# Optimization experiments

Measured on AMD Instinct MI355X. Metric: run time of the kernel, lower is better.

The kernel has to match this reference:

```python
import jax, jax.numpy as jnp
import numpy as np

N, E, F, H, K = 20000, 640000, 128, 128, 2


def setup_inputs() -> dict:
    key = jax.random.key(0)
    ks = jax.random.split(key, 8)
    x = jax.random.normal(ks[0], (N, F), jnp.float32)
    src = jax.random.randint(ks[1], (E,), 0, N)
    dst = jax.random.randint(ks[2], (E,), 0, N)
    edge_weight = jax.random.uniform(ks[3], (E,), jnp.float32)
    h = jnp.zeros((N, H), jnp.float32)
    c = jnp.zeros((N, H), jnp.float32)
    Wx = jax.random.normal(ks[4], (4, K, F, H), jnp.float32) * 0.05
    Wh = jax.random.normal(ks[5], (4, K, H, H), jnp.float32) * 0.05
    b = jnp.zeros((4, H), jnp.float32)
    wc = jax.random.normal(ks[6], (3, H), jnp.float32) * 0.05
    return dict(x=x, edge_weight=edge_weight, h=h, c=c, Wx=Wx, Wh=Wh, b=b, wc=wc,
                src=src, dst=dst)


def _lhat(x, src, dst, w_sym, n):
    # Scaled Laplacian (sym norm, lambda_max=2): L_hat = L - I = -D^-1/2 A D^-1/2
    return -jax.ops.segment_sum(w_sym[:, None] * x[src], dst, num_segments=n)


def _cheb(x, W, src, dst, w_sym, n):
    # Chebyshev recursion: T0=x, T1=L_hat x, Tk = 2 L_hat T_{k-1} - T_{k-2}
    Tx0 = x
    out = Tx0 @ W[0]
    if W.shape[0] > 1:
        Tx1 = _lhat(x, src, dst, w_sym, n)
        out = out + Tx1 @ W[1]
        for k in range(2, W.shape[0]):
            Tx2 = 2.0 * _lhat(Tx1, src, dst, w_sym, n) - Tx0
            out = out + Tx2 @ W[k]
            Tx0, Tx1 = Tx1, Tx2
    return out


def reference(x, edge_weight, h, c, Wx, Wh, b, wc, src, dst):
    n = x.shape[0]
    # symmetric normalization of edge weights
    deg = jax.ops.segment_sum(edge_weight, src, num_segments=n)
    dis = jnp.where(deg > 0, jax.lax.rsqrt(jnp.maximum(deg, 1e-12)), 0.0)
    w_sym = dis[src] * edge_weight * dis[dst]

    gx = lambda W: _cheb(x, W, src, dst, w_sym, n)
    gh = lambda W: _cheb(h, W, src, dst, w_sym, n)

    i = jax.nn.sigmoid(gx(Wx[0]) + gh(Wh[0]) + wc[0] * c + b[0])
    f = jax.nn.sigmoid(gx(Wx[1]) + gh(Wh[1]) + wc[1] * c + b[1])
    c_new = f * c + i * jnp.tanh(gx(Wx[2]) + gh(Wh[2]) + b[2])
    o = jax.nn.sigmoid(gx(Wx[3]) + gh(Wh[3]) + wc[2] * c_new + b[3])
    h_new = o * jnp.tanh(c_new)
    # module returns (out, h, c) with out == new hidden state
    return h_new, h_new, c_new
```

## Files before the change

### kernel.cpp

```cpp
#include <hip/hip_runtime.h>
#include <math.h>

#define FD 128
#define GATES 4
#define NB   128
#define NRH  2
#define NRF  2
#define RSH_MAX 10016
#define RSF_MAX 10016
#define NMAX (RSH_MAX * 2)

typedef __attribute__((ext_vector_type(8))) short bf16x8;
typedef __attribute__((ext_vector_type(4))) float f32x4;

__device__ __forceinline__ float sigmoidf_(float v) {
    return 1.0f / (1.0f + expf(-v));
}

__device__ __forceinline__ unsigned short f2bf(float f) {
    unsigned int u = __builtin_bit_cast(unsigned int, f);
    u += 0x7fffu + ((u >> 16) & 1u);
    return (unsigned short)(u >> 16);
}
__device__ __forceinline__ float bflo(unsigned int u) {
    return __builtin_bit_cast(float, u << 16);
}
__device__ __forceinline__ float bfhi(unsigned int u) {
    return __builtin_bit_cast(float, u & 0xffff0000u);
}
__device__ __forceinline__ unsigned int pack2bf(float lo, float hi) {
    return (unsigned int)f2bf(lo) | ((unsigned int)f2bf(hi) << 16);
}

__global__ __launch_bounds__(512) void k_front(
    const float* __restrict__ ew, const int* __restrict__ src,
    const int* __restrict__ dst,
    float* __restrict__ deg_priv, unsigned short* __restrict__ cnt_priv,
    int* __restrict__ cursor, int* __restrict__ hflag,
    const float* __restrict__ x, const float* __restrict__ h,
    const float* __restrict__ Wx, const float* __restrict__ Wh,
    unsigned int* __restrict__ xw, unsigned int* __restrict__ hw,
    unsigned short* __restrict__ Abf, unsigned short* __restrict__ Wbf,
    int* __restrict__ flagpart,
    int E, int n, int ech, int rs, int n16, int cvb) {

    __shared__ float        degL[RSH_MAX];
    __shared__ unsigned int cntP[RSH_MAX / 2];

    const int bid  = blockIdx.x;
    const int tid  = threadIdx.x;
    const int lane = tid & 63;
    const int NH_BLOCKS = NB * NRH;

    if (bid < NH_BLOCKS) {
        if (bid == 0 && tid == 0) { cursor[0] = 0; hflag[0] = 0; }

        const int b    = bid & (NB - 1);
        const int r    = bid >> 7;
        const int base = r * rs;
        const int rse  = min(rs, n - base);
        const int nh   = (rse + 1) >> 1;

        for (int i = tid; i < rse; i += 512) degL[i] = 0.f;
        for (int i = tid; i < nh;  i += 512) cntP[i] = 0u;
        __syncthreads();

        const int e0 = b * ech, e1 = min(e0 + ech, E);
        for (int e = e0 + tid; e < e1; e += 512) {
            int s = src[e], d = dst[e];
            unsigned int rs_ = (unsigned int)(s - base);
            unsigned int rd_ = (unsigned int)(d - base);
            if (rs_ < (unsigned int)rse) atomicAdd(&degL[rs_], ew[e]);
            if (rd_ < (unsigned int)rse) atomicAdd(&cntP[rd_ >> 1], (rd_ & 1) ? 0x10000u : 1u);
        }
        __syncthreads();

        float*          dp = deg_priv + (size_t)b * n + base;
        unsigned short* cp = cnt_priv + (size_t)b * n + base;
        for (int i = tid; i < rse; i += 512) dp[i] = degL[i];
        for (int i = tid; i < rse; i += 512) {
            unsigned int v = cntP[i >> 1];
            cp[i] = (unsigned short)((i & 1) ? (v >> 16) : (v & 0xffffu));
        }
        return;
    }

    if (bid < NH_BLOCKS + cvb) {
        int t = (bid - NH_BLOCKS) * 512 + tid;
        bool nz = false;
        if (t < n16) {
            int r = t >> 4, o = t & 15;
            int slot = ((r & 15) + 16 * (o & 3)) * 8;
            size_t fb = ((size_t)(r >> 4) * 16) * 512;

            const float4* xp = reinterpret_cast<const float4*>(x) + (size_t)t * 2;
            float4 a = xp[0], bq = xp[1];
            uint4 ox;
            ox.x = pack2bf(a.x, a.y);   ox.y = pack2bf(a.z, a.w);
            ox.z = pack2bf(bq.x, bq.y); ox.w = pack2bf(bq.z, bq.w);
            reinterpret_cast<uint4*>(xw)[t] = ox;
            *reinterpret_cast<uint4*>(Abf + fb + (size_t)(o >> 2) * 512 + slot) = ox;

            const float4* hp = reinterpret_cast<const float4*>(h) + (size_t)t * 2;
            float4 hc = hp[0], hd = hp[1];
            nz = (hc.x != 0.f) | (hc.y != 0.f) | (hc.z != 0.f) | (hc.w != 0.f) |
                 (hd.x != 0.f) | (hd.y != 0.f) | (hd.z != 0.f) | (hd.w != 0.f);
            uint4 oh;
            oh.x = pack2bf(hc.x, hc.y); oh.y = pack2bf(hc.z, hc.w);
            oh.z = pack2bf(hd.x, hd.y); oh.w = pack2bf(hd.z, hd.w);
            reinterpret_cast<uint4*>(hw)[t] = oh;
            *reinterpret_cast<uint4*>(Abf + fb + (size_t)(8 + (o >> 2)) * 512 + slot) = oh;
        }
        __shared__ int fsh;
        if (tid == 0) fsh = 0;
        __syncthreads();
        unsigned long long m = __ballot(nz);
        if (lane == 0 && m) atomicOr(&fsh, 1);
        __syncthreads();
        if (tid == 0) flagpart[bid - NH_BLOCKS] = fsh;
        return;
    }

    {
        int frag = (bid - NH_BLOCKS - cvb) * 8 + (tid >> 6);
        int cb = frag >> 4, kb = frag & 15;
        int col = cb * 16 + (lane & 15);
        int k0  = kb * 32 + (lane >> 4) * 8;

        int sel  = k0 >> 7;
        int g    = col >> 7;
        int j    = col & (FD - 1);
        const float* Wb = (sel < 2) ? Wx : Wh;
        const float* p = Wb + (((size_t)g * 2 + (sel & 1)) * FD + (k0 & (FD - 1))) * FD + j;

        unsigned short outv[8];
        #pragma unroll
        for (int i = 0; i < 8; ++i) outv[i] = f2bf(p[(size_t)i * FD]);
        *reinterpret_cast<uint4*>(Wbf + (size_t)frag * 512 + lane * 8) =
            *reinterpret_cast<uint4*>(outv);
    }
}

__global__ __launch_bounds__(512) void k_fold(
    const float* __restrict__ deg_priv, const unsigned short* __restrict__ cnt_priv,
    float* __restrict__ dis, int* __restrict__ cnt, int* __restrict__ off,
    int* __restrict__ curb, int* __restrict__ cursor, int n) {

    __shared__ float degp[4][128];
    __shared__ int   ctp[4][128];
    __shared__ int   offL[128];

    const int tid = threadIdx.x;
    const int seg = tid >> 7;
    const int dl  = tid & 127;
    const int d   = blockIdx.x * 128 + dl;
    const int b0  = seg * 32;

    float s = 0.f; int ct = 0;
    if (d < n) {
        #pragma unroll 8
        for (int i = 0; i < 32; ++i) {
            int b = b0 + i;
            s  += deg_priv[(size_t)b * n + d];
            ct += (int)cnt_priv[(size_t)b * n + d];
        }
    }
    degp[seg][dl] = s;
    ctp[seg][dl]  = ct;
    __syncthreads();

    if (seg == 0) {
        int   ctt = 0;
        float st  = 0.f;
        #pragma unroll
        for (int q = 0; q < 4; ++q) { ctt += ctp[q][dl]; st += degp[q][dl]; }

        const int lane = tid & 63;
        int s_incl = (d < n) ? ctt : 0;
        #pragma unroll
        for (int o = 1; o < 64; o <<= 1) {
            int t2 = __shfl_up(s_incl, o);
            if (lane >= o) s_incl += t2;
        }
        int wtotal = __shfl(s_incl, 63);
        int base = 0;
        if (lane == 0) base = atomicAdd(cursor, wtotal);
        base = __shfl(base, 0);

        if (d < n) {
            dis[d] = (st > 0.0f) ? rsqrtf(fmaxf(st, 1e-12f)) : 0.0f;
            cnt[d] = ctt;
            int my0 = base + s_incl - ((d < n) ? ctt : 0);
            off[d]   = my0;
            offL[dl] = my0;
        }
    }
    __syncthreads();

    if (d < n) {
        int run = offL[dl];
        for (int q = 0; q < seg; ++q) run += ctp[q][dl];
        #pragma unroll 8
        for (int i = 0; i < 32; ++i) {
            int b = b0 + i;
            curb[(size_t)b * n + d] = run;
            run += (int)cnt_priv[(size_t)b * n + d];
        }
    }
}

__global__ __launch_bounds__(512) void k_fill_lds(
    const float* __restrict__ ew, const int* __restrict__ src,
    const int* __restrict__ dst, const float* __restrict__ dis,
    const int* __restrict__ curb, int2* __restrict__ epk,
    const int* __restrict__ flagpart, int* __restrict__ hflag,
    int E, int n, int ech, int rs, int cvb) {

    __shared__ int curL[RSF_MAX];

    const int b    = blockIdx.x & (NB - 1);
    const int r    = blockIdx.x >> 7;
    const int base = r * rs;
    const int rse  = min(rs, n - base);

    if (blockIdx.x == 0) {
        int fl = 0;
        for (int i = threadIdx.x; i < cvb; i += 512) fl |= flagpart[i];
        unsigned long long m = __ballot(fl != 0);
        if ((threadIdx.x & 63) == 0 && m) atomicOr(hflag, 1);
    }

    const int* crow = curb + (size_t)b * n + base;
    for (int i = threadIdx.x; i < rse; i += 512) curL[i] = crow[i];
    __syncthreads();

    const int e0 = b * ech, e1 = min(e0 + ech, E);
    for (int e = e0 + (int)threadIdx.x; e < e1; e += 512) {
        int d = dst[e];
        unsigned int rd_ = (unsigned int)(d - base);
        if (rd_ < (unsigned int)rse) {
            int s = src[e];
            float w = -dis[s] * ew[e] * dis[d];
            int p = atomicAdd(&curL[rd_], 1);
            epk[p] = make_int2(s, __builtin_bit_cast(int, w));
        }
    }
}

__global__ __launch_bounds__(256) void k_gather_bf(
    const unsigned int* __restrict__ xw, const unsigned int* __restrict__ hw,
    const int* __restrict__ off, const int* __restrict__ cntv,
    const int2* __restrict__ epk, const int* __restrict__ hflag,
    unsigned short* __restrict__ Abf, int n) {

    int d    = blockIdx.x * 4 + (threadIdx.x >> 6);
    int lane = threadIdx.x & 63;
    if (d >= n) return;
    const bool hasH = (*hflag) != 0;

    int p0 = off[d], p1 = p0 + cntv[d];
    float ax0 = 0.f, ax1 = 0.f, ah0 = 0.f, ah1 = 0.f;

    if (!hasH) {
        for (int base = p0; base < p1; base += 64) {
            int cnt = min(64, p1 - base);
            int2 my = make_int2(0, 0);
            if (lane < cnt) my = epk[base + lane];
            int   sm = my.x;
            float wm = __builtin_bit_cast(float, my.y);
            int k = 0;
            for (; k + 4 <= cnt; k += 4) {
                int   s0 = __shfl(sm, k),     s1 = __shfl(sm, k + 1);
                int   s2 = __shfl(sm, k + 2), s3 = __shfl(sm, k + 3);
                float w0 = __shfl(wm, k),     w1 = __shfl(wm, k + 1);
                float w2 = __shfl(wm, k + 2), w3 = __shfl(wm, k + 3);
                unsigned int u0 = xw[s0 * 64 + lane];
                unsigned int u1 = xw[s1 * 64 + lane];
                unsigned int u2 = xw[s2 * 64 + lane];
                unsigned int u3 = xw[s3 * 64 + lane];
                ax0 = fmaf(w0, bflo(u0), ax0); ax1 = fmaf(w0, bfhi(u0), ax1);
                ax0 = fmaf(w1, bflo(u1), ax0); ax1 = fmaf(w1, bfhi(u1), ax1);
                ax0 = fmaf(w2, bflo(u2), ax0); ax1 = fmaf(w2, bfhi(u2), ax1);
                ax0 = fmaf(w3, bflo(u3), ax0); ax1 = fmaf(w3, bfhi(u3), ax1);
            }
            for (; k < cnt; ++k) {
                int s = __shfl(sm, k);
                float w = __shfl(wm, k);
                unsigned int u = xw[s * 64 + lane];
                ax0 = fmaf(w, bflo(u), ax0); ax1 = fmaf(w, bfhi(u), ax1);
            }
        }
    } else {
        for (int base = p0; base < p1; base += 64) {
            int cnt = min(64, p1 - base);
            int2 my = make_int2(0, 0);
            if (lane < cnt) my = epk[base + lane];
            int   sm = my.x;
            float wm = __builtin_bit_cast(float, my.y);
            int k = 0;
            for (; k + 2 <= cnt; k += 2) {
                int   s0 = __shfl(sm, k), s1 = __shfl(sm, k + 1);
                float w0 = __shfl(wm, k), w1 = __shfl(wm, k + 1);
                unsigned int u0 = xw[s0 * 64 + lane];
                unsigned int v0 = hw[s0 * 64 + lane];
                unsigned int u1 = xw[s1 * 64 + lane];
                unsigned int v1 = hw[s1 * 64 + lane];
                ax0 = fmaf(w0, bflo(u0), ax0); ax1 = fmaf(w0, bfhi(u0), ax1);
                ah0 = fmaf(w0, bflo(v0), ah0); ah1 = fmaf(w0, bfhi(v0), ah1);
                ax0 = fmaf(w1, bflo(u1), ax0); ax1 = fmaf(w1, bfhi(u1), ax1);
                ah0 = fmaf(w1, bflo(v1), ah0); ah1 = fmaf(w1, bfhi(v1), ah1);
            }
            for (; k < cnt; ++k) {
                int s = __shfl(sm, k);
                float w = __shfl(wm, k);
                unsigned int u = xw[s * 64 + lane];
                unsigned int v = hw[s * 64 + lane];
                ax0 = fmaf(w, bflo(u), ax0); ax1 = fmaf(w, bfhi(u), ax1);
                ah0 = fmaf(w, bflo(v), ah0); ah1 = fmaf(w, bfhi(v), ah1);
            }
        }
    }

    unsigned int* Au = (unsigned int*)Abf;
    size_t fragT = (size_t)(d >> 4) * 16 + 4 + (lane >> 4);
    int slotu = ((d & 15) + 16 * ((lane >> 2) & 3)) * 4 + (lane & 3);
    Au[fragT * 256 + slotu] = pack2bf(ax0, ax1);
    if (hasH) Au[(fragT + 8) * 256 + slotu] = pack2bf(ah0, ah1);
}

__global__ __launch_bounds__(512) void k_gemm_lstm(
    const unsigned short* __restrict__ Abf, const unsigned short* __restrict__ Wbf,
    const int* __restrict__ hflag,
    const float* __restrict__ c, const float* __restrict__ bias,
    const float* __restrict__ wc, float* __restrict__ out, int n) {

    int rt   = blockIdx.x;
    int jj   = threadIdx.x >> 6;
    int lane = threadIdx.x & 63;
    const int kbmax = (*hflag) ? 16 : 8;

    f32x4 acc[4][4];
    #pragma unroll
    for (int mi = 0; mi < 4; ++mi)
        #pragma unroll
        for (int g = 0; g < 4; ++g)
            acc[mi][g] = (f32x4)0.0f;

    const size_t aoff = ((size_t)(rt * 4) * 16) * 512 + lane * 8;

    for (int kb = 0; kb < kbmax; ++kb) {
        bf16x8 a[4], b[4];
        #pragma unroll
        for (int mi = 0; mi < 4; ++mi)
            a[mi] = *reinterpret_cast<const bf16x8*>(Abf + aoff + (size_t)(mi * 16 + kb) * 512);
        #pragma unroll
        for (int g = 0; g < 4; ++g)
            b[g] = *reinterpret_cast<const bf16x8*>(
                Wbf + ((size_t)(g * 8 + jj) * 16 + kb) * 512 + lane * 8);
        #pragma unroll
        for (int mi = 0; mi < 4; ++mi)
            #pragma unroll
            for (int g = 0; g < 4; ++g)
                acc[mi][g] = __builtin_amdgcn_mfma_f32_16x16x32_bf16(
                                 a[mi], b[g], acc[mi][g], 0, 0, 0);
    }

    const int r0   = rt * 64;
    const int col  = jj * 16 + (lane & 15);
    const size_t NH = (size_t)n * FD;
    const float wc0 = wc[0 * FD + col], wc1 = wc[1 * FD + col], wc2 = wc[2 * FD + col];
    const float b0  = bias[0 * FD + col], b1 = bias[1 * FD + col];
    const float b2  = bias[2 * FD + col], b3 = bias[3 * FD + col];

    #pragma unroll
    for (int mi = 0; mi < 4; ++mi) {
        #pragma unroll
        for (int q = 0; q < 4; ++q) {
            int r = r0 + mi * 16 + (lane >> 4) * 4 + q;
            if (r >= n) continue;
            float cv = c[(size_t)r * FD + col];
            float gi = acc[mi][0][q] + wc0 * cv + b0;
            float gf = acc[mi][1][q] + wc1 * cv + b1;
            float gg = acc[mi][2][q] + b2;
            float iv = sigmoidf_(gi);
            float fv = sigmoidf_(gf);
            float cn = fv * cv + iv * tanhf(gg);
            float go = acc[mi][3][q] + wc2 * cn + b3;
            float hn = sigmoidf_(go) * tanhf(cn);
            size_t o = (size_t)r * FD + col;
            out[o]          = hn;
            out[NH + o]     = hn;
            out[2 * NH + o] = cn;
        }
    }
}

extern "C" void kernel_launch(void* const* d_in, const int* in_sizes, int n_in,
                              void* d_out, int out_size, void* d_ws, size_t ws_size,
                              hipStream_t stream) {
    const float* x   = (const float*)d_in[0];
    const float* ew  = (const float*)d_in[1];
    const float* h   = (const float*)d_in[2];
    const float* c   = (const float*)d_in[3];
    const float* Wx  = (const float*)d_in[4];
    const float* Wh  = (const float*)d_in[5];
    const float* b   = (const float*)d_in[6];
    const float* wc  = (const float*)d_in[7];
    const int*   src = (const int*)d_in[8];
    const int*   dst = (const int*)d_in[9];

    const int n = in_sizes[0] / FD;
    const int E = in_sizes[1];

    const int Mpad = (n + 63) & ~63;
    const int ech  = (E + NB - 1) / NB;
    const int rsh  = (n + NRH - 1) / NRH;
    const int rsf  = (n + NRF - 1) / NRF;
    const int n16  = n * 16;
    const int cvb  = (n16 + 511) / 512;
    const int npf  = (n + 127) / 128;

    float* dis      = (float*)d_ws;
    int*   cnt      = (int*)(dis + n);
    int*   off      = cnt + n;
    int*   hflag    = off + n + 4;
    int*   cursor   = hflag + 4;
    int*   flagpart = cursor + 4;
    int2*  epk      = (int2*)(flagpart + 1280);
    unsigned int* xw = (unsigned int*)(epk + E);
    unsigned int* hw = xw + (size_t)n * 64;
    unsigned short* Abf = (unsigned short*)(hw + (size_t)n * 64);
    unsigned short* Wbf = Abf + (size_t)Mpad * 512;
    int*   curb     = (int*)(Wbf + 512 * 512);
    float* deg_priv = (float*)(curb + (size_t)NB * n);
    unsigned short* cnt_priv = (unsigned short*)(deg_priv + (size_t)NB * n);

    k_front<<<NB * NRH + cvb + 64, 512, 0, stream>>>(
        ew, src, dst, deg_priv, cnt_priv, cursor, hflag,
        x, h, Wx, Wh, xw, hw, Abf, Wbf, flagpart,
        E, n, ech, rsh, n16, cvb);
    k_fold<<<npf, 512, 0, stream>>>(deg_priv, cnt_priv, dis, cnt, off, curb,
                                    cursor, n);
    k_fill_lds<<<NB * NRF, 512, 0, stream>>>(ew, src, dst, dis, curb, epk,
                                             flagpart, hflag, E, n, ech, rsf, cvb);
    k_gather_bf<<<(n + 3) / 4, 256, 0, stream>>>(xw, hw, off, cnt, epk, hflag, Abf, n);

    k_gemm_lstm<<<Mpad / 64, 512, 0, stream>>>(Abf, Wbf, hflag, c, b, wc,
                                               (float*)d_out, n);
}
```

Measured before the change: 95.13 us.

## Stage GEMM A operand through LDS from row-major bf16 buffers

```diff
diff --git a/kernel.cpp b/kernel.cpp
--- a/kernel.cpp
+++ b/kernel.cpp
@@ -9,6 +9,7 @@
 #define RSH_MAX 10016
 #define RSF_MAX 10016
 #define NMAX (RSH_MAX * 2)
+#define LDW 68
 
 typedef __attribute__((ext_vector_type(8))) short bf16x8;
 typedef __attribute__((ext_vector_type(4))) float f32x4;
@@ -40,8 +41,7 @@
     const float* __restrict__ x, const float* __restrict__ h,
     const float* __restrict__ Wx, const float* __restrict__ Wh,
     unsigned int* __restrict__ xw, unsigned int* __restrict__ hw,
-    unsigned short* __restrict__ Abf, unsigned short* __restrict__ Wbf,
-    int* __restrict__ flagpart,
+    unsigned short* __restrict__ Wbf, int* __restrict__ flagpart,
     int E, int n, int ech, int rs, int n16, int cvb) {
 
     __shared__ float        degL[RSH_MAX];
@@ -66,7 +66,21 @@
         __syncthreads();
 
         const int e0 = b * ech, e1 = min(e0 + ech, E);
-        for (int e = e0 + tid; e < e1; e += 512) {
+        int e = e0 + tid * 2;
+        for (; e + 1 < e1; e += 1024) {
+            int2   s2 = *reinterpret_cast<const int2*>(src + e);
+            int2   d2 = *reinterpret_cast<const int2*>(dst + e);
+            float2 w2 = *reinterpret_cast<const float2*>(ew + e);
+            unsigned int rs0 = (unsigned int)(s2.x - base);
+            unsigned int rd0 = (unsigned int)(d2.x - base);
+            unsigned int rs1 = (unsigned int)(s2.y - base);
+            unsigned int rd1 = (unsigned int)(d2.y - base);
+            if (rs0 < (unsigned int)rse) atomicAdd(&degL[rs0], w2.x);
+            if (rd0 < (unsigned int)rse) atomicAdd(&cntP[rd0 >> 1], (rd0 & 1) ? 0x10000u : 1u);
+            if (rs1 < (unsigned int)rse) atomicAdd(&degL[rs1], w2.y);
+            if (rd1 < (unsigned int)rse) atomicAdd(&cntP[rd1 >> 1], (rd1 & 1) ? 0x10000u : 1u);
+        }
+        if (e < e1) {
             int s = src[e], d = dst[e];
             unsigned int rs_ = (unsigned int)(s - base);
             unsigned int rd_ = (unsigned int)(d - base);
@@ -89,17 +103,12 @@
         int t = (bid - NH_BLOCKS) * 512 + tid;
         bool nz = false;
         if (t < n16) {
-            int r = t >> 4, o = t & 15;
-            int slot = ((r & 15) + 16 * (o & 3)) * 8;
-            size_t fb = ((size_t)(r >> 4) * 16) * 512;
-
             const float4* xp = reinterpret_cast<const float4*>(x) + (size_t)t * 2;
             float4 a = xp[0], bq = xp[1];
             uint4 ox;
             ox.x = pack2bf(a.x, a.y);   ox.y = pack2bf(a.z, a.w);
             ox.z = pack2bf(bq.x, bq.y); ox.w = pack2bf(bq.z, bq.w);
             reinterpret_cast<uint4*>(xw)[t] = ox;
-            *reinterpret_cast<uint4*>(Abf + fb + (size_t)(o >> 2) * 512 + slot) = ox;
 
             const float4* hp = reinterpret_cast<const float4*>(h) + (size_t)t * 2;
             float4 hc = hp[0], hd = hp[1];
@@ -109,7 +118,6 @@
             oh.x = pack2bf(hc.x, hc.y); oh.y = pack2bf(hc.z, hc.w);
             oh.z = pack2bf(hd.x, hd.y); oh.w = pack2bf(hd.z, hd.w);
             reinterpret_cast<uint4*>(hw)[t] = oh;
-            *reinterpret_cast<uint4*>(Abf + fb + (size_t)(8 + (o >> 2)) * 512 + slot) = oh;
         }
         __shared__ int fsh;
         if (tid == 0) fsh = 0;
@@ -190,7 +198,7 @@
         if (d < n) {
             dis[d] = (st > 0.0f) ? rsqrtf(fmaxf(st, 1e-12f)) : 0.0f;
             cnt[d] = ctt;
-            int my0 = base + s_incl - ((d < n) ? ctt : 0);
+            int my0 = base + s_incl - ctt;
             off[d]   = my0;
             offL[dl] = my0;
         }
@@ -235,7 +243,25 @@
     __syncthreads();
 
     const int e0 = b * ech, e1 = min(e0 + ech, E);
-    for (int e = e0 + (int)threadIdx.x; e < e1; e += 512) {
+    int e = e0 + (int)threadIdx.x * 2;
+    for (; e + 1 < e1; e += 1024) {
+        int2   s2 = *reinterpret_cast<const int2*>(src + e);
+        int2   d2 = *reinterpret_cast<const int2*>(dst + e);
+        float2 w2 = *reinterpret_cast<const float2*>(ew + e);
+        unsigned int rd0 = (unsigned int)(d2.x - base);
+        if (rd0 < (unsigned int)rse) {
+            float w = -dis[s2.x] * w2.x * dis[d2.x];
+            int p = atomicAdd(&curL[rd0], 1);
+            epk[p] = make_int2(s2.x, __builtin_bit_cast(int, w));
+        }
+        unsigned int rd1 = (unsigned int)(d2.y - base);
+        if (rd1 < (unsigned int)rse) {
+            float w = -dis[s2.y] * w2.y * dis[d2.y];
+            int p = atomicAdd(&curL[rd1], 1);
+            epk[p] = make_int2(s2.y, __builtin_bit_cast(int, w));
+        }
+    }
+    if (e < e1) {
         int d = dst[e];
         unsigned int rd_ = (unsigned int)(d - base);
         if (rd_ < (unsigned int)rse) {
@@ -251,7 +277,7 @@
     const unsigned int* __restrict__ xw, const unsigned int* __restrict__ hw,
     const int* __restrict__ off, const int* __restrict__ cntv,
     const int2* __restrict__ epk, const int* __restrict__ hflag,
-    unsigned short* __restrict__ Abf, int n) {
+    unsigned int* __restrict__ txw, unsigned int* __restrict__ thw, int n) {
 
     int d    = blockIdx.x * 4 + (threadIdx.x >> 6);
     int lane = threadIdx.x & 63;
@@ -290,6 +316,7 @@
                 ax0 = fmaf(w, bflo(u), ax0); ax1 = fmaf(w, bfhi(u), ax1);
             }
         }
+        txw[(size_t)d * 64 + lane] = pack2bf(ax0, ax1);
     } else {
         for (int base = p0; base < p1; base += 64) {
             int cnt = min(64, p1 - base);
@@ -319,25 +346,27 @@
                 ah0 = fmaf(w, bflo(v), ah0); ah1 = fmaf(w, bfhi(v), ah1);
             }
         }
-    }
-
-    unsigned int* Au = (unsigned int*)Abf;
-    size_t fragT = (size_t)(d >> 4) * 16 + 4 + (lane >> 4);
-    int slotu = ((d & 15) + 16 * ((lane >> 2) & 3)) * 4 + (lane & 3);
-    Au[fragT * 256 + slotu] = pack2bf(ax0, ax1);
-    if (hasH) Au[(fragT + 8) * 256 + slotu] = pack2bf(ah0, ah1);
+        txw[(size_t)d * 64 + lane] = pack2bf(ax0, ax1);
+        thw[(size_t)d * 64 + lane] = pack2bf(ah0, ah1);
+    }
 }
 
 __global__ __launch_bounds__(512) void k_gemm_lstm(
-    const unsigned short* __restrict__ Abf, const unsigned short* __restrict__ Wbf,
-    const int* __restrict__ hflag,
+    const unsigned int* __restrict__ xw, const unsigned int* __restrict__ txw,
+    const unsigned int* __restrict__ hw, const unsigned int* __restrict__ thw,
+    const unsigned short* __restrict__ Wbf, const int* __restrict__ hflag,
     const float* __restrict__ c, const float* __restrict__ bias,
     const float* __restrict__ wc, float* __restrict__ out, int n) {
 
-    int rt   = blockIdx.x;
-    int jj   = threadIdx.x >> 6;
-    int lane = threadIdx.x & 63;
-    const int kbmax = (*hflag) ? 16 : 8;
+    __shared__ unsigned int ldsR[64][LDW];
+    __shared__ unsigned int ldsG[64][LDW];
+
+    const int rt   = blockIdx.x;
+    const int tid  = threadIdx.x;
+    const int jj   = tid >> 6;
+    const int lane = tid & 63;
+    const int r0   = rt * 64;
+    const bool hasH = (*hflag) != 0;
 
     f32x4 acc[4][4];
     #pragma unroll
@@ -346,13 +375,33 @@
         for (int g = 0; g < 4; ++g)
             acc[mi][g] = (f32x4)0.0f;
 
-    const size_t aoff = ((size_t)(rt * 4) * 16) * 512 + lane * 8;
-
-    for (int kb = 0; kb < kbmax; ++kb) {
+    {
+        int sr = tid >> 3, sc = (tid & 7) * 8;
+        uint4 v0 = make_uint4(0,0,0,0), v1 = make_uint4(0,0,0,0);
+        uint4 g0 = make_uint4(0,0,0,0), g1 = make_uint4(0,0,0,0);
+        if (r0 + sr < n) {
+            const uint4* p = reinterpret_cast<const uint4*>(xw + (size_t)(r0 + sr) * 64 + sc);
+            v0 = p[0]; v1 = p[1];
+            const uint4* q = reinterpret_cast<const uint4*>(txw + (size_t)(r0 + sr) * 64 + sc);
+            g0 = q[0]; g1 = q[1];
+        }
+        *reinterpret_cast<uint4*>(&ldsR[sr][sc])     = v0;
+        *reinterpret_cast<uint4*>(&ldsR[sr][sc + 4]) = v1;
+        *reinterpret_cast<uint4*>(&ldsG[sr][sc])     = g0;
+        *reinterpret_cast<uint4*>(&ldsG[sr][sc + 4]) = g1;
+    }
+    __syncthreads();
+
+    #pragma unroll
+    for (int kb = 0; kb < 8; ++kb) {
         bf16x8 a[4], b[4];
-        #pragma unroll
-        for (int mi = 0; mi < 4; ++mi)
-            a[mi] = *reinterpret_cast<const bf16x8*>(Abf + aoff + (size_t)(mi * 16 + kb) * 512);
+        const int c0 = (kb & 3) * 16 + (lane >> 4) * 4;
+        #pragma unroll
+        for (int mi = 0; mi < 4; ++mi) {
+            const unsigned int* lp = (kb < 4) ? &ldsR[mi * 16 + (lane & 15)][c0]
+                                              : &ldsG[mi * 16 + (lane & 15)][c0];
+            a[mi] = __builtin_bit_cast(bf16x8, *reinterpret_cast<const uint4*>(lp));
+        }
         #pragma unroll
         for (int g = 0; g < 4; ++g)
             b[g] = *reinterpret_cast<const bf16x8*>(
@@ -365,7 +414,49 @@
                                  a[mi], b[g], acc[mi][g], 0, 0, 0);
     }
 
-    const int r0   = rt * 64;
+    if (hasH) {
+        __syncthreads();
+        {
+            int sr = tid >> 3, sc = (tid & 7) * 8;
+            uint4 v0 = make_uint4(0,0,0,0), v1 = make_uint4(0,0,0,0);
+            uint4 g0 = make_uint4(0,0,0,0), g1 = make_uint4(0,0,0,0);
+            if (r0 + sr < n) {
+                const uint4* p = reinterpret_cast<const uint4*>(hw + (size_t)(r0 + sr) * 64 + sc);
+                v0 = p[0]; v1 = p[1];
+                const uint4* q = reinterpret_cast<const uint4*>(thw + (size_t)(r0 + sr) * 64 + sc);
+                g0 = q[0]; g1 = q[1];
+            }
+            *reinterpret_cast<uint4*>(&ldsR[sr][sc])     = v0;
+            *reinterpret_cast<uint4*>(&ldsR[sr][sc + 4]) = v1;
+            *reinterpret_cast<uint4*>(&ldsG[sr][sc])     = g0;
+            *reinterpret_cast<uint4*>(&ldsG[sr][sc + 4]) = g1;
+        }
+        __syncthreads();
+
+        #pragma unroll
+        for (int kk = 0; kk < 8; ++kk) {
+            const int kb = 8 + kk;
+            bf16x8 a[4], b[4];
+            const int c0 = (kk & 3) * 16 + (lane >> 4) * 4;
+            #pragma unroll
+            for (int mi = 0; mi < 4; ++mi) {
+                const unsigned int* lp = (kk < 4) ? &ldsR[mi * 16 + (lane & 15)][c0]
+                                                  : &ldsG[mi * 16 + (lane & 15)][c0];
+                a[mi] = __builtin_bit_cast(bf16x8, *reinterpret_cast<const uint4*>(lp));
+            }
+            #pragma unroll
+            for (int g = 0; g < 4; ++g)
+                b[g] = *reinterpret_cast<const bf16x8*>(
+                    Wbf + ((size_t)(g * 8 + jj) * 16 + kb) * 512 + lane * 8);
+            #pragma unroll
+            for (int mi = 0; mi < 4; ++mi)
+                #pragma unroll
+                for (int g = 0; g < 4; ++g)
+                    acc[mi][g] = __builtin_amdgcn_mfma_f32_16x16x32_bf16(
+                                     a[mi], b[g], acc[mi][g], 0, 0, 0);
+        }
+    }
+
     const int col  = jj * 16 + (lane & 15);
     const size_t NH = (size_t)n * FD;
     const float wc0 = wc[0 * FD + col], wc1 = wc[1 * FD + col], wc2 = wc[2 * FD + col];
@@ -427,24 +518,25 @@
     int*   cursor   = hflag + 4;
     int*   flagpart = cursor + 4;
     int2*  epk      = (int2*)(flagpart + 1280);
-    unsigned int* xw = (unsigned int*)(epk + E);
-    unsigned int* hw = xw + (size_t)n * 64;
-    unsigned short* Abf = (unsigned short*)(hw + (size_t)n * 64);
-    unsigned short* Wbf = Abf + (size_t)Mpad * 512;
+    unsigned int* xw  = (unsigned int*)(epk + E);
+    unsigned int* hw  = xw + (size_t)n * 64;
+    unsigned int* txw = hw + (size_t)n * 64;
+    unsigned int* thw = txw + (size_t)n * 64;
+    unsigned short* Wbf = (unsigned short*)(thw + (size_t)n * 64);
     int*   curb     = (int*)(Wbf + 512 * 512);
     float* deg_priv = (float*)(curb + (size_t)NB * n);
     unsigned short* cnt_priv = (unsigned short*)(deg_priv + (size_t)NB * n);
 
     k_front<<<NB * NRH + cvb + 64, 512, 0, stream>>>(
         ew, src, dst, deg_priv, cnt_priv, cursor, hflag,
-        x, h, Wx, Wh, xw, hw, Abf, Wbf, flagpart,
+        x, h, Wx, Wh, xw, hw, Wbf, flagpart,
         E, n, ech, rsh, n16, cvb);
     k_fold<<<npf, 512, 0, stream>>>(deg_priv, cnt_priv, dis, cnt, off, curb,
                                     cursor, n);
     k_fill_lds<<<NB * NRF, 512, 0, stream>>>(ew, src, dst, dis, curb, epk,
                                              flagpart, hflag, E, n, ech, rsf, cvb);
-    k_gather_bf<<<(n + 3) / 4, 256, 0, stream>>>(xw, hw, off, cnt, epk, hflag, Abf, n);
-
-    k_gemm_lstm<<<Mpad / 64, 512, 0, stream>>>(Abf, Wbf, hflag, c, b, wc,
-                                               (float*)d_out, n);
-}
+    k_gather_bf<<<(n + 3) / 4, 256, 0, stream>>>(xw, hw, off, cnt, epk, hflag,
+                                                 txw, thw, n);
+    k_gemm_lstm<<<Mpad / 64, 512, 0, stream>>>(xw, txw, hw, thw, Wbf, hflag,
+                                               c, b, wc, (float*)d_out, n);
+}
```

Measured after the change: 93.11 us. 2.1% less time.
